# Optimization experiments

Hardware: AMD Instinct MI355X
Metric: run time of the kernel (lower is better)

Reference implementation:

```python
import jax, jax.numpy as jnp
import numpy as np

R_GAS = 8314.46261815324   # Cantera gas constant, J/(kmol K)
ONE_ATM = 101325.0
B, S, NR = 2048, 100, 800
POLY = 5


def setup_inputs() -> dict:
    key = jax.random.key(0)
    ks = jax.random.split(key, 11)
    T = jax.random.uniform(ks[0], (B, 1), minval=300.0, maxval=2500.0)
    P = ONE_ATM * jax.random.uniform(ks[1], (B, 1), minval=0.5, maxval=2.0)
    Y = jax.random.uniform(ks[2], (B, S), minval=0.01, maxval=1.0)
    TPY = jnp.concatenate([T, P, Y], axis=1)
    molecular_weights = jax.random.uniform(ks[3], (S, 1), minval=2.0, maxval=100.0)
    # NASA-7 coefficients with realistic per-column magnitudes
    scales = jnp.array([1.0, 1e-3, 1e-6, 1e-9, 1e-12, 1e3, 1.0])
    base = jnp.array([3.5, 0.0, 0.0, 0.0, 0.0, 0.0, 5.0])
    nasa_low = jax.random.normal(ks[4], (S, 7)) * scales + base
    nasa_high = jax.random.normal(ks[5], (S, 7)) * scales + base
    efficiencies_coeffs = jax.random.uniform(ks[6], (S, NR), minval=0.0, maxval=2.0)
    is_three_body = (jax.random.uniform(ks[7], (NR,)) < 0.3).astype(jnp.float32)
    # positive poly coefficients so viscosity/conductivity/diffusion stay > 0
    species_viscosities_poly = jax.random.uniform(ks[8], (POLY, S), minval=1e-6, maxval=1e-5)
    thermal_conductivity_poly = jax.random.uniform(ks[9], (POLY, S), minval=1e-4, maxval=1e-3)
    binary_diff_coeffs_poly = jax.random.uniform(ks[10], (POLY, S * S), minval=1e-7, maxval=1e-6)
    return {
        'TPY': TPY,
        'molecular_weights': molecular_weights,
        'nasa_low': nasa_low,
        'nasa_high': nasa_high,
        'efficiencies_coeffs': efficiencies_coeffs,
        'is_three_body': is_three_body,
        'species_viscosities_poly': species_viscosities_poly,
        'thermal_conductivity_poly': thermal_conductivity_poly,
        'binary_diff_coeffs_poly': binary_diff_coeffs_poly,
    }


def _forward(TPY, mw, nasa_low, nasa_high, eff, i3b, visc_poly, cond_poly, bdiff_poly):
    n_sp = mw.shape[0]
    # ---- set_states: state variables ----
    T = jnp.clip(TPY[:, 0:1], 200.0, None)            # [B,1]
    logT = jnp.log(T)
    P = TPY[:, 1:2]
    Y = jnp.clip(TPY[:, 2:], 0.0, None)
    Y = Y / Y.sum(axis=1, keepdims=True)
    mean_W = 1.0 / (Y @ (1.0 / mw))                   # [B,1]
    rho = P / R_GAS / T * mean_W                      # mass density
    X = Y * mean_W / mw.T                             # mole fractions
    C = Y * rho / mw.T                                # molar concentrations
    mask = (T <= 1000.0).astype(T.dtype)              # [B,1] NASA branch select
    # ---- cp (NASA poly) ----
    cp_T = jnp.concatenate([T**0, T, T**2, T**3, T**4], axis=1)
    cp = (cp_T @ nasa_low[:, :5].T) * mask + (cp_T @ nasa_high[:, :5].T) * (1.0 - mask)
    cp_mole = (R_GAS * cp * X).sum(axis=1)
    # ---- enthalpy ----
    H_T = jnp.concatenate([T**0, T / 2, T**2 / 3, T**3 / 4, T**4 / 5, 1.0 / T], axis=1)
    H = ((H_T @ nasa_low[:, :6].T) * mask + (H_T @ nasa_high[:, :6].T) * (1.0 - mask)) * R_GAS * T
    h = H / mw.T
    enthalpy_mass = (h * Y).sum(axis=1)
    # ---- entropy ----
    idx = jnp.array([0, 1, 2, 3, 4, 6])
    S_T = jnp.concatenate([logT, T, T**2 / 2, T**3 / 3, T**4 / 4, T**0], axis=1)
    S0 = ((S_T @ nasa_low[:, idx].T) * mask + (S_T @ nasa_high[:, idx].T) * (1.0 - mask)) * R_GAS
    S_sp = S0 - R_GAS * jnp.log(X) - R_GAS * jnp.log(P / ONE_ATM)
    s = S_sp / mw.T
    entropy_mass = (s * Y).sum(axis=1)
    # ---- third-body effective concentrations ----
    C_M = C @ eff                                     # [B,NR]
    C_M2 = C_M * i3b + (1.0 - i3b)
    # ---- update_transport: viscosity (Wilke mixing) ----
    poly_order = visc_poly.shape[0]
    trans_T = jnp.concatenate([logT**i for i in range(poly_order - 1, -1, -1)], axis=1)
    sp_visc = trans_T @ visc_poly                     # [B,S]
    Wk_over_Wj = mw @ (1.0 / mw.T)                    # [S,S]
    Wj_over_Wk = 1.0 / Wk_over_Wj
    eta_ratio = sp_visc[:, :, None] / sp_visc[:, None, :]  # [B,S,S]
    PHI = (1.0 / 2.8284271247461903) / jnp.sqrt(1.0 + Wk_over_Wj) \
          * (1.0 + jnp.sqrt(eta_ratio) * Wj_over_Wk**0.25) ** 2
    denom = jnp.einsum('bij,bj->bi', PHI, X)
    viscosities = (X * sp_visc / denom).sum(axis=1, keepdims=True)
    # ---- thermal conductivity ----
    sp_cond = trans_T @ cond_poly
    thermal_conductivity = 0.5 * ((X * sp_cond).sum(axis=1, keepdims=True)
                                  + 1.0 / (X / sp_cond).sum(axis=1, keepdims=True))
    # ---- mixture-averaged diffusion coefficients ----
    bdc = (trans_T @ bdiff_poly).reshape(-1, n_sp, n_sp)    # [B,S,S]
    X_eps = jnp.clip(X, 1e-12, None)
    XjWj = X_eps @ mw - X_eps * mw.T                        # [B,S]
    XjDjk = jnp.einsum('bj,bjk->bk', X_eps, 1.0 / bdc) \
            - X_eps / jnp.diagonal(bdc, axis1=-2, axis2=-1)
    mix_diff = XjWj / XjDjk / mean_W / P * ONE_ATM
    return jnp.concatenate([cp_mole[:, None], enthalpy_mass[:, None], entropy_mass[:, None],
                            C_M2, viscosities, thermal_conductivity, mix_diff], axis=1)


def reference(TPY, molecular_weights, nasa_low, nasa_high, efficiencies_coeffs,
              is_three_body, species_viscosities_poly, thermal_conductivity_poly,
              binary_diff_coeffs_poly):
    return _forward(TPY, molecular_weights, nasa_low, nasa_high, efficiencies_coeffs,
                    is_three_body, species_viscosities_poly, thermal_conductivity_poly,
                    binary_diff_coeffs_poly)
```

## Files before the change

### kernel.cpp

```cpp
#include <hip/hip_runtime.h>
#include <math.h>

namespace {

constexpr int S = 100;
constexpr int NR = 800;
constexpr int RPB = 8;
constexpr int NTH = 512;
constexpr int IN_COLS = 2 + S;
constexpr int OUT_COLS = 3 + NR + 2 + S;
constexpr float RGASF = 8314.46261815324f;
constexpr float ATMF = 101325.0f;

__device__ __forceinline__ float wave_sum(float v) {
#pragma unroll
  for (int off = 32; off; off >>= 1) v += __shfl_xor(v, off);
  return v;
}

__global__ __launch_bounds__(NTH)
void chem_props_kernel(const float* __restrict__ TPY,
                       const float* __restrict__ mw,
                       const float* __restrict__ nasa_low,
                       const float* __restrict__ nasa_high,
                       const float* __restrict__ eff,
                       const float* __restrict__ i3b,
                       const float* __restrict__ visc_poly,
                       const float* __restrict__ cond_poly,
                       const float* __restrict__ bdiff_poly,
                       float* __restrict__ out)
{
  __shared__ __align__(16) float Xl[S][RPB];
  __shared__ __align__(16) float u1l[S][RPB];
  __shared__ __align__(16) float u2l[S][RPB];
  __shared__ __align__(16) float viscl[S][RPB];
  __shared__ __align__(16) float svl[S][RPB];
  __shared__ __align__(16) float denoml[S][RPB];
  __shared__ __align__(16) float xjdl[S][RPB];
  __shared__ float mwl[S], imwl[S];
  __shared__ float rs_L[RPB], rs_cfac[RPB], rs_mW[RPB], rs_scale[RPB];
  __shared__ float vsum[RPB];

  const int tid = threadIdx.x;
  const int wid = tid >> 6;
  const int lane = tid & 63;
  const int row0 = blockIdx.x * RPB;
  const int rowg = row0 + wid;

  for (int idx = tid; idx < S * RPB; idx += NTH) {
    (&denoml[0][0])[idx] = 0.0f;
    (&xjdl[0][0])[idx] = 0.0f;
  }
  if (tid < RPB) vsum[tid] = 0.0f;
  if (tid < S) {
    float m = mw[tid];
    mwl[tid] = m;
    imwl[tid] = 1.0f / m;
  }
  __syncthreads();

  {
    const float* rowp = TPY + (size_t)rowg * IN_COLS;
    float T = fmaxf(rowp[0], 200.0f);
    float P = rowp[1];
    float L = logf(T);
    float T2 = T * T, T3 = T2 * T, T4 = T2 * T2;
    float invT = 1.0f / T;

    int sA = lane, sB = lane + 64;
    bool hasB = (sB < S);
    float y0 = fmaxf(rowp[2 + sA], 0.0f);
    float y1 = hasB ? fmaxf(rowp[2 + sB], 0.0f) : 0.0f;
    float im0 = imwl[sA];
    float im1 = hasB ? imwl[sB] : 0.0f;

    float ysum = wave_sum(y0 + y1);
    float invy = 1.0f / ysum;
    float sw = wave_sum(y0 * im0 + y1 * im1) * invy;
    float mW = 1.0f / sw;
    float cfac = P / (RGASF * T);
    float lnP = logf(P * (1.0f / ATMF));

    const float* nasa = (T <= 1000.0f) ? nasa_low : nasa_high;

    float cpx = 0.0f, hy = 0.0f, sy = 0.0f, condA = 0.0f, condB = 0.0f;
#pragma unroll
    for (int t = 0; t < 2; ++t) {
      int s = (t == 0) ? sA : sB;
      if (s < S) {
        float yn = ((t == 0) ? y0 : y1) * invy;
        float im = (t == 0) ? im0 : im1;
        float x = fmaxf(yn * mW * im, 1e-12f);
        const float* a = nasa + s * 7;
        float a0 = a[0], a1 = a[1], a2 = a[2], a3 = a[3],
              a4 = a[4], a5 = a[5], a6 = a[6];
        float cp = a0 + a1 * T + a2 * T2 + a3 * T3 + a4 * T4;
        float Ht = a0 + 0.5f * a1 * T + (1.0f / 3.0f) * a2 * T2
                 + 0.25f * a3 * T3 + 0.2f * a4 * T4 + a5 * invT;
        float S0r = a0 * L + a1 * T + 0.5f * a2 * T2
                  + (1.0f / 3.0f) * a3 * T3 + 0.25f * a4 * T4 + a6;
        cpx += cp * x;
        hy += Ht * im * yn;
        sy += (S0r - logf(x) - lnP) * im * yn;

        float v = visc_poly[0 * S + s];
        v = fmaf(v, L, visc_poly[1 * S + s]);
        v = fmaf(v, L, visc_poly[2 * S + s]);
        v = fmaf(v, L, visc_poly[3 * S + s]);
        v = fmaf(v, L, visc_poly[4 * S + s]);
        float c = cond_poly[0 * S + s];
        c = fmaf(c, L, cond_poly[1 * S + s]);
        c = fmaf(c, L, cond_poly[2 * S + s]);
        c = fmaf(c, L, cond_poly[3 * S + s]);
        c = fmaf(c, L, cond_poly[4 * S + s]);
        condA += x * c;
        condB += x / c;
        float sv = sqrtf(v);
        Xl[s][wid] = x;
        viscl[s][wid] = v;
        svl[s][wid] = sv;
        u1l[s][wid] = x / sv;
        u2l[s][wid] = x / v;
      }
    }
    float scp = wave_sum(cpx);
    float sh = wave_sum(hy);
    float ss = wave_sum(sy);
    float sca = wave_sum(condA);
    float scb = wave_sum(condB);
    if (lane == 0) {
      float* orow = out + (size_t)rowg * OUT_COLS;
      orow[0] = RGASF * scp;
      orow[1] = RGASF * T * sh;
      orow[2] = RGASF * ss;
      orow[3 + NR + 1] = 0.5f * (sca + 1.0f / scb);
      rs_L[wid] = L;
      rs_cfac[wid] = cfac;
      rs_mW[wid] = mW;
      rs_scale[wid] = ATMF / (mW * P);
    }
  }
  __syncthreads();

  for (int q = tid; q < NR; q += NTH) {
    float acc[RPB];
#pragma unroll
    for (int b = 0; b < RPB; ++b) acc[b] = 0.0f;
    for (int s = 0; s < S; ++s) {
      float e = eff[s * NR + q];
      float xv[RPB];
      *(float4*)&xv[0] = *(const float4*)&Xl[s][0];
      *(float4*)&xv[4] = *(const float4*)&Xl[s][4];
#pragma unroll
      for (int b = 0; b < RPB; ++b) acc[b] = fmaf(xv[b], e, acc[b]);
    }
    float t3 = i3b[q];
    float base = 1.0f - t3;
#pragma unroll
    for (int b = 0; b < RPB; ++b) {
      float cm = acc[b] * rs_cfac[b];
      out[(size_t)(row0 + b) * OUT_COLS + 3 + q] = fmaf(cm, t3, base);
    }
  }

  if (tid < 500) {
    const int i = tid % 100;
    const int kg = tid / 100;
    const float mwi = mwl[i];
    const float imwi = imwl[i];
    float d0[RPB], d1[RPB], d2[RPB];
#pragma unroll
    for (int b = 0; b < RPB; ++b) { d0[b] = 0; d1[b] = 0; d2[b] = 0; }
    const int k0 = kg * 20;
    for (int k = k0; k < k0 + 20; ++k) {
      float mwk = mwl[k];
      float A = 0.35355339059327373f *
                __builtin_amdgcn_rsqf(1.0f + mwi * imwl[k]);
      float B4 = sqrtf(sqrtf(mwk * imwi));
      float m1 = A * B4, m2 = m1 * B4;
      float xv[RPB], u1v[RPB], u2v[RPB];
      *(float4*)&xv[0] = *(const float4*)&Xl[k][0];
      *(float4*)&xv[4] = *(const float4*)&Xl[k][4];
      *(float4*)&u1v[0] = *(const float4*)&u1l[k][0];
      *(float4*)&u1v[4] = *(const float4*)&u1l[k][4];
      *(float4*)&u2v[0] = *(const float4*)&u2l[k][0];
      *(float4*)&u2v[4] = *(const float4*)&u2l[k][4];
#pragma unroll
      for (int b = 0; b < RPB; ++b) {
        d0[b] = fmaf(A, xv[b], d0[b]);
        d1[b] = fmaf(m1, u1v[b], d1[b]);
        d2[b] = fmaf(m2, u2v[b], d2[b]);
      }
    }
#pragma unroll
    for (int b = 0; b < RPB; ++b) {
      float pden = d0[b] + 2.0f * svl[i][b] * d1[b] + viscl[i][b] * d2[b];
      atomicAdd(&denoml[i][b], pden);
    }
  }
  __syncthreads();

  if (tid < 800) {
    const int i = tid % 100;
    const int b = tid / 100;
    float contrib = Xl[i][b] * viscl[i][b] / denoml[i][b];
    atomicAdd(&vsum[b], contrib);
  }
  if (tid < 500) {
    const int k = tid % 100;
    const int jg = tid / 100;
    float Lb[RPB];
#pragma unroll
    for (int b = 0; b < RPB; ++b) Lb[b] = rs_L[b];
    float acc[RPB];
#pragma unroll
    for (int b = 0; b < RPB; ++b) acc[b] = 0.0f;
    const int j0 = jg * 20;
    for (int j = j0; j < j0 + 20; ++j) {
      if (j == k) continue;
      float c0 = bdiff_poly[0 * 10000 + j * 100 + k];
      float c1 = bdiff_poly[1 * 10000 + j * 100 + k];
      float c2 = bdiff_poly[2 * 10000 + j * 100 + k];
      float c3 = bdiff_poly[3 * 10000 + j * 100 + k];
      float c4 = bdiff_poly[4 * 10000 + j * 100 + k];
      float xv[RPB];
      *(float4*)&xv[0] = *(const float4*)&Xl[j][0];
      *(float4*)&xv[4] = *(const float4*)&Xl[j][4];
#pragma unroll
      for (int b = 0; b < RPB; ++b) {
        float p = fmaf(c0, Lb[b], c1);
        p = fmaf(p, Lb[b], c2);
        p = fmaf(p, Lb[b], c3);
        p = fmaf(p, Lb[b], c4);
        acc[b] = fmaf(xv[b], __builtin_amdgcn_rcpf(p), acc[b]);
      }
    }
#pragma unroll
    for (int b = 0; b < RPB; ++b) atomicAdd(&xjdl[k][b], acc[b]);
  }
  __syncthreads();

  if (tid < RPB) {
    out[(size_t)(row0 + tid) * OUT_COLS + 3 + NR] = vsum[tid];
  }
  if (tid < 800) {
    const int k = tid % 100;
    const int b = tid / 100;
    float num = rs_mW[b] - Xl[k][b] * mwl[k];
    float md = num / xjdl[k][b] * rs_scale[b];
    out[(size_t)(row0 + b) * OUT_COLS + 3 + NR + 2 + k] = md;
  }
}

}

extern "C" void kernel_launch(void* const* d_in, const int* in_sizes, int n_in,
                              void* d_out, int out_size, void* d_ws, size_t ws_size,
                              hipStream_t stream) {
  const float* TPY        = (const float*)d_in[0];
  const float* mwp        = (const float*)d_in[1];
  const float* nasa_low   = (const float*)d_in[2];
  const float* nasa_high  = (const float*)d_in[3];
  const float* eff        = (const float*)d_in[4];
  const float* i3b        = (const float*)d_in[5];
  const float* visc_poly  = (const float*)d_in[6];
  const float* cond_poly  = (const float*)d_in[7];
  const float* bdiff_poly = (const float*)d_in[8];
  float* out = (float*)d_out;

  const int B = 2048;
  dim3 grid(B / RPB);
  chem_props_kernel<<<grid, NTH, 0, stream>>>(
      TPY, mwp, nasa_low, nasa_high, eff, i3b,
      visc_poly, cond_poly, bdiff_poly, out);
}
```

Baseline: 111.5 us.

## Halve rows per block and split species across two waves per row

Rows per block drop from 8 to 4, which doubles the grid, and each row's 100 species are split across two waves whose partial sums are combined through shared memory. The third-body loop gives each thread two adjacent reactions and reads them with float2 loads; fast __logf intrinsics and small unroll pragmas are also added. The aim is better CU occupancy and latency hiding, since the old launch had about one block per CU. The cost is that the efficiency matrix and poly tables are re-read by twice as many blocks, there are extra syncs, and __logf is slightly less accurate.

```diff
diff --git a/kernel.cpp b/kernel.cpp
--- a/kernel.cpp
+++ b/kernel.cpp
@@ -5,7 +5,7 @@
 
 constexpr int S = 100;
 constexpr int NR = 800;
-constexpr int RPB = 8;
+constexpr int RPB = 4;
 constexpr int NTH = 512;
 constexpr int IN_COLS = 2 + S;
 constexpr int OUT_COLS = 3 + NR + 2 + S;
@@ -38,14 +38,15 @@
   __shared__ __align__(16) float denoml[S][RPB];
   __shared__ __align__(16) float xjdl[S][RPB];
   __shared__ float mwl[S], imwl[S];
-  __shared__ float rs_L[RPB], rs_cfac[RPB], rs_mW[RPB], rs_scale[RPB];
+  __shared__ float pa[8][2];
+  __shared__ float pb[8][5];
+  __shared__ float rs_L[RPB], rs_cfac[RPB], rs_mW[RPB], rs_scale[RPB], rs_T[RPB];
   __shared__ float vsum[RPB];
 
   const int tid = threadIdx.x;
   const int wid = tid >> 6;
   const int lane = tid & 63;
   const int row0 = blockIdx.x * RPB;
-  const int rowg = row0 + wid;
 
   for (int idx = tid; idx < S * RPB; idx += NTH) {
     (&denoml[0][0])[idx] = 0.0f;
@@ -60,68 +61,68 @@
   __syncthreads();
 
   {
+    const int row = wid & 3;
+    const int half = wid >> 2;
+    const int rowg = row0 + row;
     const float* rowp = TPY + (size_t)rowg * IN_COLS;
     float T = fmaxf(rowp[0], 200.0f);
     float P = rowp[1];
-    float L = logf(T);
+    float L = __logf(T);
     float T2 = T * T, T3 = T2 * T, T4 = T2 * T2;
     float invT = 1.0f / T;
 
-    int sA = lane, sB = lane + 64;
-    bool hasB = (sB < S);
-    float y0 = fmaxf(rowp[2 + sA], 0.0f);
-    float y1 = hasB ? fmaxf(rowp[2 + sB], 0.0f) : 0.0f;
-    float im0 = imwl[sA];
-    float im1 = hasB ? imwl[sB] : 0.0f;
-
-    float ysum = wave_sum(y0 + y1);
+    int s = half * 64 + lane;
+    bool valid = (s < S);
+    float y = valid ? fmaxf(rowp[2 + s], 0.0f) : 0.0f;
+    float im = valid ? imwl[s] : 0.0f;
+
+    float py = wave_sum(y);
+    float pw = wave_sum(y * im);
+    if (lane == 0) { pa[wid][0] = py; pa[wid][1] = pw; }
+    __syncthreads();
+    float ysum = pa[row][0] + pa[row + 4][0];
+    float wsum = pa[row][1] + pa[row + 4][1];
     float invy = 1.0f / ysum;
-    float sw = wave_sum(y0 * im0 + y1 * im1) * invy;
-    float mW = 1.0f / sw;
+    float mW = ysum / wsum;
     float cfac = P / (RGASF * T);
-    float lnP = logf(P * (1.0f / ATMF));
+    float lnP = __logf(P * (1.0f / ATMF));
 
     const float* nasa = (T <= 1000.0f) ? nasa_low : nasa_high;
 
     float cpx = 0.0f, hy = 0.0f, sy = 0.0f, condA = 0.0f, condB = 0.0f;
-#pragma unroll
-    for (int t = 0; t < 2; ++t) {
-      int s = (t == 0) ? sA : sB;
-      if (s < S) {
-        float yn = ((t == 0) ? y0 : y1) * invy;
-        float im = (t == 0) ? im0 : im1;
-        float x = fmaxf(yn * mW * im, 1e-12f);
-        const float* a = nasa + s * 7;
-        float a0 = a[0], a1 = a[1], a2 = a[2], a3 = a[3],
-              a4 = a[4], a5 = a[5], a6 = a[6];
-        float cp = a0 + a1 * T + a2 * T2 + a3 * T3 + a4 * T4;
-        float Ht = a0 + 0.5f * a1 * T + (1.0f / 3.0f) * a2 * T2
-                 + 0.25f * a3 * T3 + 0.2f * a4 * T4 + a5 * invT;
-        float S0r = a0 * L + a1 * T + 0.5f * a2 * T2
-                  + (1.0f / 3.0f) * a3 * T3 + 0.25f * a4 * T4 + a6;
-        cpx += cp * x;
-        hy += Ht * im * yn;
-        sy += (S0r - logf(x) - lnP) * im * yn;
-
-        float v = visc_poly[0 * S + s];
-        v = fmaf(v, L, visc_poly[1 * S + s]);
-        v = fmaf(v, L, visc_poly[2 * S + s]);
-        v = fmaf(v, L, visc_poly[3 * S + s]);
-        v = fmaf(v, L, visc_poly[4 * S + s]);
-        float c = cond_poly[0 * S + s];
-        c = fmaf(c, L, cond_poly[1 * S + s]);
-        c = fmaf(c, L, cond_poly[2 * S + s]);
-        c = fmaf(c, L, cond_poly[3 * S + s]);
-        c = fmaf(c, L, cond_poly[4 * S + s]);
-        condA += x * c;
-        condB += x / c;
-        float sv = sqrtf(v);
-        Xl[s][wid] = x;
-        viscl[s][wid] = v;
-        svl[s][wid] = sv;
-        u1l[s][wid] = x / sv;
-        u2l[s][wid] = x / v;
-      }
+    if (valid) {
+      float yn = y * invy;
+      float x = fmaxf(yn * mW * im, 1e-12f);
+      const float* a = nasa + s * 7;
+      float a0 = a[0], a1 = a[1], a2 = a[2], a3 = a[3],
+            a4 = a[4], a5 = a[5], a6 = a[6];
+      float cp = a0 + a1 * T + a2 * T2 + a3 * T3 + a4 * T4;
+      float Ht = a0 + 0.5f * a1 * T + (1.0f / 3.0f) * a2 * T2
+               + 0.25f * a3 * T3 + 0.2f * a4 * T4 + a5 * invT;
+      float S0r = a0 * L + a1 * T + 0.5f * a2 * T2
+                + (1.0f / 3.0f) * a3 * T3 + 0.25f * a4 * T4 + a6;
+      cpx = cp * x;
+      hy = Ht * im * yn;
+      sy = (S0r - __logf(x) - lnP) * im * yn;
+
+      float v = visc_poly[0 * S + s];
+      v = fmaf(v, L, visc_poly[1 * S + s]);
+      v = fmaf(v, L, visc_poly[2 * S + s]);
+      v = fmaf(v, L, visc_poly[3 * S + s]);
+      v = fmaf(v, L, visc_poly[4 * S + s]);
+      float c = cond_poly[0 * S + s];
+      c = fmaf(c, L, cond_poly[1 * S + s]);
+      c = fmaf(c, L, cond_poly[2 * S + s]);
+      c = fmaf(c, L, cond_poly[3 * S + s]);
+      c = fmaf(c, L, cond_poly[4 * S + s]);
+      condA = x * c;
+      condB = x / c;
+      float sv = sqrtf(v);
+      Xl[s][row] = x;
+      viscl[s][row] = v;
+      svl[s][row] = sv;
+      u1l[s][row] = x / sv;
+      u2l[s][row] = x / v;
     }
     float scp = wave_sum(cpx);
     float sh = wave_sum(hy);
@@ -129,37 +130,57 @@
     float sca = wave_sum(condA);
     float scb = wave_sum(condB);
     if (lane == 0) {
-      float* orow = out + (size_t)rowg * OUT_COLS;
-      orow[0] = RGASF * scp;
-      orow[1] = RGASF * T * sh;
-      orow[2] = RGASF * ss;
-      orow[3 + NR + 1] = 0.5f * (sca + 1.0f / scb);
-      rs_L[wid] = L;
-      rs_cfac[wid] = cfac;
-      rs_mW[wid] = mW;
-      rs_scale[wid] = ATMF / (mW * P);
-    }
-  }
-  __syncthreads();
-
-  for (int q = tid; q < NR; q += NTH) {
-    float acc[RPB];
-#pragma unroll
-    for (int b = 0; b < RPB; ++b) acc[b] = 0.0f;
+      pb[wid][0] = scp; pb[wid][1] = sh; pb[wid][2] = ss;
+      pb[wid][3] = sca; pb[wid][4] = scb;
+      if (half == 0) {
+        rs_L[row] = L;
+        rs_T[row] = T;
+        rs_cfac[row] = cfac;
+        rs_mW[row] = mW;
+        rs_scale[row] = ATMF / (mW * P);
+      }
+    }
+  }
+  __syncthreads();
+
+  if (tid < RPB) {
+    const int row = tid;
+    float scp = pb[row][0] + pb[row + 4][0];
+    float sh  = pb[row][1] + pb[row + 4][1];
+    float ss  = pb[row][2] + pb[row + 4][2];
+    float sca = pb[row][3] + pb[row + 4][3];
+    float scb = pb[row][4] + pb[row + 4][4];
+    float* orow = out + (size_t)(row0 + row) * OUT_COLS;
+    orow[0] = RGASF * scp;
+    orow[1] = RGASF * rs_T[row] * sh;
+    orow[2] = RGASF * ss;
+    orow[3 + NR + 1] = 0.5f * (sca + 1.0f / scb);
+  }
+
+  if (tid < 400) {
+    const int q0 = 2 * tid;
+    float acc[2 * RPB];
+#pragma unroll
+    for (int b = 0; b < 2 * RPB; ++b) acc[b] = 0.0f;
+#pragma unroll 4
     for (int s = 0; s < S; ++s) {
-      float e = eff[s * NR + q];
+      float2 e = *(const float2*)&eff[s * NR + q0];
       float xv[RPB];
       *(float4*)&xv[0] = *(const float4*)&Xl[s][0];
-      *(float4*)&xv[4] = *(const float4*)&Xl[s][4];
-#pragma unroll
-      for (int b = 0; b < RPB; ++b) acc[b] = fmaf(xv[b], e, acc[b]);
-    }
-    float t3 = i3b[q];
-    float base = 1.0f - t3;
+#pragma unroll
+      for (int b = 0; b < RPB; ++b) {
+        acc[b] = fmaf(xv[b], e.x, acc[b]);
+        acc[RPB + b] = fmaf(xv[b], e.y, acc[RPB + b]);
+      }
+    }
+    float2 t3 = *(const float2*)&i3b[q0];
+    float base0 = 1.0f - t3.x, base1 = 1.0f - t3.y;
 #pragma unroll
     for (int b = 0; b < RPB; ++b) {
-      float cm = acc[b] * rs_cfac[b];
-      out[(size_t)(row0 + b) * OUT_COLS + 3 + q] = fmaf(cm, t3, base);
+      float cf = rs_cfac[b];
+      float* op = out + (size_t)(row0 + b) * OUT_COLS + 3 + q0;
+      op[0] = fmaf(acc[b] * cf, t3.x, base0);
+      op[1] = fmaf(acc[RPB + b] * cf, t3.y, base1);
     }
   }
 
@@ -172,6 +193,7 @@
 #pragma unroll
     for (int b = 0; b < RPB; ++b) { d0[b] = 0; d1[b] = 0; d2[b] = 0; }
     const int k0 = kg * 20;
+#pragma unroll 2
     for (int k = k0; k < k0 + 20; ++k) {
       float mwk = mwl[k];
       float A = 0.35355339059327373f *
@@ -180,11 +202,8 @@
       float m1 = A * B4, m2 = m1 * B4;
       float xv[RPB], u1v[RPB], u2v[RPB];
       *(float4*)&xv[0] = *(const float4*)&Xl[k][0];
-      *(float4*)&xv[4] = *(const float4*)&Xl[k][4];
       *(float4*)&u1v[0] = *(const float4*)&u1l[k][0];
-      *(float4*)&u1v[4] = *(const float4*)&u1l[k][4];
       *(float4*)&u2v[0] = *(const float4*)&u2l[k][0];
-      *(float4*)&u2v[4] = *(const float4*)&u2l[k][4];
 #pragma unroll
       for (int b = 0; b < RPB; ++b) {
         d0[b] = fmaf(A, xv[b], d0[b]);
@@ -200,7 +219,7 @@
   }
   __syncthreads();
 
-  if (tid < 800) {
+  if (tid < 100 * RPB) {
     const int i = tid % 100;
     const int b = tid / 100;
     float contrib = Xl[i][b] * viscl[i][b] / denoml[i][b];
@@ -216,6 +235,7 @@
 #pragma unroll
     for (int b = 0; b < RPB; ++b) acc[b] = 0.0f;
     const int j0 = jg * 20;
+#pragma unroll 2
     for (int j = j0; j < j0 + 20; ++j) {
       if (j == k) continue;
       float c0 = bdiff_poly[0 * 10000 + j * 100 + k];
@@ -225,7 +245,6 @@
       float c4 = bdiff_poly[4 * 10000 + j * 100 + k];
       float xv[RPB];
       *(float4*)&xv[0] = *(const float4*)&Xl[j][0];
-      *(float4*)&xv[4] = *(const float4*)&Xl[j][4];
 #pragma unroll
       for (int b = 0; b < RPB; ++b) {
         float p = fmaf(c0, Lb[b], c1);
@@ -243,7 +262,7 @@
   if (tid < RPB) {
     out[(size_t)(row0 + tid) * OUT_COLS + 3 + NR] = vsum[tid];
   }
-  if (tid < 800) {
+  if (tid < 100 * RPB) {
     const int k = tid % 100;
     const int b = tid / 100;
     float num = rs_mW[b] - Xl[k][b] * mwl[k];
```

New measurement: 105.4 us. -5.4%, faster.

## Split fused kernel into per-row stage and job-specialized worker blocks

Applied to the files above, without the earlier changes.

Replaces the single monolithic kernel with two launches. A stage kernel computes the per-row thermo state and writes X, viscosity and related terms to the workspace. A worker kernel then launches seven specialized blocks per 8-row tile: four for the three-body efficiencies matmul, one for the viscosity denominator, and two for diffusion halves. The aim is more parallelism and occupancy, since each block now does one job instead of running phases serially. The cost is a workspace round trip, an extra launch, and redundant X loads. It also uses fast intrinsics (__logf, exp2-based fourth root, rcp/rsq approximations), which may change accuracy slightly.

```diff
diff --git a/kernel.cpp b/kernel.cpp
--- a/kernel.cpp
+++ b/kernel.cpp
@@ -5,250 +5,304 @@
 
 constexpr int S = 100;
 constexpr int NR = 800;
-constexpr int RPB = 8;
-constexpr int NTH = 512;
+constexpr int RPT = 8;
 constexpr int IN_COLS = 2 + S;
 constexpr int OUT_COLS = 3 + NR + 2 + S;
 constexpr float RGASF = 8314.46261815324f;
 constexpr float ATMF = 101325.0f;
 
+constexpr size_t OFF_X  = 0;
+constexpr size_t OFF_U1 = 204800;
+constexpr size_t OFF_U2 = 409600;
+constexpr size_t OFF_V  = 614400;
+constexpr size_t OFF_RS = 819200;
+
 __device__ __forceinline__ float wave_sum(float v) {
 #pragma unroll
   for (int off = 32; off; off >>= 1) v += __shfl_xor(v, off);
   return v;
 }
 
-__global__ __launch_bounds__(NTH)
-void chem_props_kernel(const float* __restrict__ TPY,
-                       const float* __restrict__ mw,
-                       const float* __restrict__ nasa_low,
-                       const float* __restrict__ nasa_high,
-                       const float* __restrict__ eff,
-                       const float* __restrict__ i3b,
-                       const float* __restrict__ visc_poly,
-                       const float* __restrict__ cond_poly,
-                       const float* __restrict__ bdiff_poly,
-                       float* __restrict__ out)
+__device__ __forceinline__ float elem(const float4& v, int i) {
+  return ((const float*)&v)[i];
+}
+
+__global__ __launch_bounds__(512)
+void stage_a_kernel(const float* __restrict__ TPY,
+                    const float* __restrict__ mw,
+                    const float* __restrict__ nasa_low,
+                    const float* __restrict__ nasa_high,
+                    const float* __restrict__ visc_poly,
+                    const float* __restrict__ cond_poly,
+                    float* __restrict__ ws,
+                    float* __restrict__ out)
 {
-  __shared__ __align__(16) float Xl[S][RPB];
-  __shared__ __align__(16) float u1l[S][RPB];
-  __shared__ __align__(16) float u2l[S][RPB];
-  __shared__ __align__(16) float viscl[S][RPB];
-  __shared__ __align__(16) float svl[S][RPB];
-  __shared__ __align__(16) float denoml[S][RPB];
-  __shared__ __align__(16) float xjdl[S][RPB];
-  __shared__ float mwl[S], imwl[S];
-  __shared__ float rs_L[RPB], rs_cfac[RPB], rs_mW[RPB], rs_scale[RPB];
-  __shared__ float vsum[RPB];
-
+  __shared__ float imw[S];
   const int tid = threadIdx.x;
   const int wid = tid >> 6;
   const int lane = tid & 63;
-  const int row0 = blockIdx.x * RPB;
-  const int rowg = row0 + wid;
-
-  for (int idx = tid; idx < S * RPB; idx += NTH) {
-    (&denoml[0][0])[idx] = 0.0f;
-    (&xjdl[0][0])[idx] = 0.0f;
-  }
-  if (tid < RPB) vsum[tid] = 0.0f;
-  if (tid < S) {
-    float m = mw[tid];
-    mwl[tid] = m;
-    imwl[tid] = 1.0f / m;
-  }
+  if (tid < S) imw[tid] = 1.0f / mw[tid];
   __syncthreads();
 
-  {
-    const float* rowp = TPY + (size_t)rowg * IN_COLS;
-    float T = fmaxf(rowp[0], 200.0f);
-    float P = rowp[1];
-    float L = logf(T);
-    float T2 = T * T, T3 = T2 * T, T4 = T2 * T2;
-    float invT = 1.0f / T;
-
-    int sA = lane, sB = lane + 64;
-    bool hasB = (sB < S);
-    float y0 = fmaxf(rowp[2 + sA], 0.0f);
-    float y1 = hasB ? fmaxf(rowp[2 + sB], 0.0f) : 0.0f;
-    float im0 = imwl[sA];
-    float im1 = hasB ? imwl[sB] : 0.0f;
-
-    float ysum = wave_sum(y0 + y1);
-    float invy = 1.0f / ysum;
-    float sw = wave_sum(y0 * im0 + y1 * im1) * invy;
-    float mW = 1.0f / sw;
-    float cfac = P / (RGASF * T);
-    float lnP = logf(P * (1.0f / ATMF));
-
-    const float* nasa = (T <= 1000.0f) ? nasa_low : nasa_high;
-
-    float cpx = 0.0f, hy = 0.0f, sy = 0.0f, condA = 0.0f, condB = 0.0f;
-#pragma unroll
-    for (int t = 0; t < 2; ++t) {
-      int s = (t == 0) ? sA : sB;
-      if (s < S) {
-        float yn = ((t == 0) ? y0 : y1) * invy;
-        float im = (t == 0) ? im0 : im1;
-        float x = fmaxf(yn * mW * im, 1e-12f);
-        const float* a = nasa + s * 7;
-        float a0 = a[0], a1 = a[1], a2 = a[2], a3 = a[3],
-              a4 = a[4], a5 = a[5], a6 = a[6];
-        float cp = a0 + a1 * T + a2 * T2 + a3 * T3 + a4 * T4;
-        float Ht = a0 + 0.5f * a1 * T + (1.0f / 3.0f) * a2 * T2
-                 + 0.25f * a3 * T3 + 0.2f * a4 * T4 + a5 * invT;
-        float S0r = a0 * L + a1 * T + 0.5f * a2 * T2
-                  + (1.0f / 3.0f) * a3 * T3 + 0.25f * a4 * T4 + a6;
-        cpx += cp * x;
-        hy += Ht * im * yn;
-        sy += (S0r - logf(x) - lnP) * im * yn;
-
-        float v = visc_poly[0 * S + s];
-        v = fmaf(v, L, visc_poly[1 * S + s]);
-        v = fmaf(v, L, visc_poly[2 * S + s]);
-        v = fmaf(v, L, visc_poly[3 * S + s]);
-        v = fmaf(v, L, visc_poly[4 * S + s]);
-        float c = cond_poly[0 * S + s];
-        c = fmaf(c, L, cond_poly[1 * S + s]);
-        c = fmaf(c, L, cond_poly[2 * S + s]);
-        c = fmaf(c, L, cond_poly[3 * S + s]);
-        c = fmaf(c, L, cond_poly[4 * S + s]);
-        condA += x * c;
-        condB += x / c;
-        float sv = sqrtf(v);
-        Xl[s][wid] = x;
-        viscl[s][wid] = v;
-        svl[s][wid] = sv;
-        u1l[s][wid] = x / sv;
-        u2l[s][wid] = x / v;
-      }
-    }
-    float scp = wave_sum(cpx);
-    float sh = wave_sum(hy);
-    float ss = wave_sum(sy);
-    float sca = wave_sum(condA);
-    float scb = wave_sum(condB);
-    if (lane == 0) {
-      float* orow = out + (size_t)rowg * OUT_COLS;
-      orow[0] = RGASF * scp;
-      orow[1] = RGASF * T * sh;
-      orow[2] = RGASF * ss;
-      orow[3 + NR + 1] = 0.5f * (sca + 1.0f / scb);
-      rs_L[wid] = L;
-      rs_cfac[wid] = cfac;
-      rs_mW[wid] = mW;
-      rs_scale[wid] = ATMF / (mW * P);
-    }
-  }
+  const int row = blockIdx.x * 8 + wid;
+  const float* rowp = TPY + (size_t)row * IN_COLS;
+  float T = fmaxf(rowp[0], 200.0f);
+  float P = rowp[1];
+  float L = __logf(T);
+  float T2 = T * T, T3 = T2 * T, T4 = T2 * T2;
+  float invT = 1.0f / T;
+
+  int sA = lane, sB = lane + 64;
+  bool hasB = (sB < S);
+  float y0 = fmaxf(rowp[2 + sA], 0.0f);
+  float y1 = hasB ? fmaxf(rowp[2 + sB], 0.0f) : 0.0f;
+  float im0 = imw[sA];
+  float im1 = hasB ? imw[sB] : 0.0f;
+
+  float ysum = wave_sum(y0 + y1);
+  float invy = 1.0f / ysum;
+  float wsum = wave_sum(y0 * im0 + y1 * im1);
+  float mW = ysum / wsum;
+  float cfac = P / (RGASF * T);
+  float lnP = __logf(P * (1.0f / ATMF));
+  const float* nasa = (T <= 1000.0f) ? nasa_low : nasa_high;
+
+  float cpx = 0.0f, hy = 0.0f, sy = 0.0f, condA = 0.0f, condB = 0.0f;
+#pragma unroll
+  for (int t = 0; t < 2; ++t) {
+    int s = t ? sB : sA;
+    if (s < S) {
+      float y = t ? y1 : y0;
+      float im = t ? im1 : im0;
+      float yn = y * invy;
+      float x = fmaxf(yn * mW * im, 1e-12f);
+      const float* a = nasa + s * 7;
+      float a0 = a[0], a1 = a[1], a2 = a[2], a3 = a[3],
+            a4 = a[4], a5 = a[5], a6 = a[6];
+      float cp = a0 + a1 * T + a2 * T2 + a3 * T3 + a4 * T4;
+      float Ht = a0 + 0.5f * a1 * T + (1.0f / 3.0f) * a2 * T2
+               + 0.25f * a3 * T3 + 0.2f * a4 * T4 + a5 * invT;
+      float S0r = a0 * L + a1 * T + 0.5f * a2 * T2
+                + (1.0f / 3.0f) * a3 * T3 + 0.25f * a4 * T4 + a6;
+      cpx += cp * x;
+      hy += Ht * im * yn;
+      sy += (S0r - __logf(x) - lnP) * im * yn;
+
+      float v = visc_poly[0 * S + s];
+      v = fmaf(v, L, visc_poly[1 * S + s]);
+      v = fmaf(v, L, visc_poly[2 * S + s]);
+      v = fmaf(v, L, visc_poly[3 * S + s]);
+      v = fmaf(v, L, visc_poly[4 * S + s]);
+      float c = cond_poly[0 * S + s];
+      c = fmaf(c, L, cond_poly[1 * S + s]);
+      c = fmaf(c, L, cond_poly[2 * S + s]);
+      c = fmaf(c, L, cond_poly[3 * S + s]);
+      c = fmaf(c, L, cond_poly[4 * S + s]);
+      condA += x * c;
+      condB += x / c;
+
+      size_t o = (size_t)row * 100 + s;
+      ws[OFF_X + o]  = x;
+      ws[OFF_V + o]  = v;
+      ws[OFF_U1 + o] = x * __builtin_amdgcn_rsqf(v);
+      ws[OFF_U2 + o] = x * __builtin_amdgcn_rcpf(v);
+    }
+  }
+  float scp = wave_sum(cpx);
+  float sh = wave_sum(hy);
+  float ss = wave_sum(sy);
+  float sca = wave_sum(condA);
+  float scb = wave_sum(condB);
+  if (lane == 0) {
+    float* orow = out + (size_t)row * OUT_COLS;
+    orow[0] = RGASF * scp;
+    orow[1] = RGASF * T * sh;
+    orow[2] = RGASF * ss;
+    orow[3 + NR + 1] = 0.5f * (sca + 1.0f / scb);
+    float* rs = ws + OFF_RS + (size_t)row * 4;
+    rs[0] = L;
+    rs[1] = cfac;
+    rs[2] = mW;
+    rs[3] = ATMF / (mW * P);
+  }
+}
+
+__global__ __launch_bounds__(256, 6)
+void worker_kernel(const float* __restrict__ eff,
+                   const float* __restrict__ i3b,
+                   const float* __restrict__ bdiff,
+                   const float* __restrict__ mw,
+                   const float* __restrict__ ws,
+                   float* __restrict__ out)
+{
+  __shared__ __align__(16) float X8[S][RPT];
+  __shared__ __align__(16) float U18[S][RPT];
+  __shared__ __align__(16) float U28[S][RPT];
+  __shared__ __align__(16) float V8[S][RPT];
+  __shared__ float rs8[RPT][4];
+  __shared__ float mwl[S], ilmx[S], ilmy[S];
+  __shared__ __align__(16) float den[S][RPT];
+  __shared__ __align__(16) float xjd[50][RPT];
+  __shared__ float psum[2][RPT];
+
+  const int t = threadIdx.x;
+  const int bid = blockIdx.x;
+  const int rt = bid / 7;
+  const int job = bid - rt * 7;
+  const int row0 = rt * RPT;
+
+  const float* wsX = ws + OFF_X + (size_t)row0 * 100;
+  for (int idx = t; idx < 800; idx += 256)
+    X8[idx % 100][idx / 100] = wsX[idx];
+  if (job == 4) {
+    const float* w1 = ws + OFF_U1 + (size_t)row0 * 100;
+    const float* w2 = ws + OFF_U2 + (size_t)row0 * 100;
+    const float* wv = ws + OFF_V + (size_t)row0 * 100;
+    for (int idx = t; idx < 800; idx += 256) {
+      U18[idx % 100][idx / 100] = w1[idx];
+      U28[idx % 100][idx / 100] = w2[idx];
+      V8[idx % 100][idx / 100] = wv[idx];
+      (&den[0][0])[idx] = 0.0f;
+    }
+  }
+  if (job >= 5 && t < 50 * RPT) (&xjd[0][0])[t] = 0.0f;
+  if (t < S) {
+    float m = mw[t];
+    mwl[t] = m;
+    ilmx[t] = 1.0f / m;
+    ilmy[t] = __log2f(m);
+  }
+  if (t < RPT * 4) (&rs8[0][0])[t] = ws[OFF_RS + (size_t)row0 * 4 + t];
   __syncthreads();
 
-  for (int q = tid; q < NR; q += NTH) {
-    float acc[RPB];
-#pragma unroll
-    for (int b = 0; b < RPB; ++b) acc[b] = 0.0f;
-    for (int s = 0; s < S; ++s) {
-      float e = eff[s * NR + q];
-      float xv[RPB];
-      *(float4*)&xv[0] = *(const float4*)&Xl[s][0];
-      *(float4*)&xv[4] = *(const float4*)&Xl[s][4];
-#pragma unroll
-      for (int b = 0; b < RPB; ++b) acc[b] = fmaf(xv[b], e, acc[b]);
-    }
-    float t3 = i3b[q];
-    float base = 1.0f - t3;
-#pragma unroll
-    for (int b = 0; b < RPB; ++b) {
-      float cm = acc[b] * rs_cfac[b];
-      out[(size_t)(row0 + b) * OUT_COLS + 3 + q] = fmaf(cm, t3, base);
-    }
-  }
-
-  if (tid < 500) {
-    const int i = tid % 100;
-    const int kg = tid / 100;
-    const float mwi = mwl[i];
-    const float imwi = imwl[i];
-    float d0[RPB], d1[RPB], d2[RPB];
-#pragma unroll
-    for (int b = 0; b < RPB; ++b) { d0[b] = 0; d1[b] = 0; d2[b] = 0; }
-    const int k0 = kg * 20;
-    for (int k = k0; k < k0 + 20; ++k) {
-      float mwk = mwl[k];
-      float A = 0.35355339059327373f *
-                __builtin_amdgcn_rsqf(1.0f + mwi * imwl[k]);
-      float B4 = sqrtf(sqrtf(mwk * imwi));
-      float m1 = A * B4, m2 = m1 * B4;
-      float xv[RPB], u1v[RPB], u2v[RPB];
-      *(float4*)&xv[0] = *(const float4*)&Xl[k][0];
-      *(float4*)&xv[4] = *(const float4*)&Xl[k][4];
-      *(float4*)&u1v[0] = *(const float4*)&u1l[k][0];
-      *(float4*)&u1v[4] = *(const float4*)&u1l[k][4];
-      *(float4*)&u2v[0] = *(const float4*)&u2l[k][0];
-      *(float4*)&u2v[4] = *(const float4*)&u2l[k][4];
-#pragma unroll
-      for (int b = 0; b < RPB; ++b) {
-        d0[b] = fmaf(A, xv[b], d0[b]);
-        d1[b] = fmaf(m1, u1v[b], d1[b]);
-        d2[b] = fmaf(m2, u2v[b], d2[b]);
-      }
-    }
-#pragma unroll
-    for (int b = 0; b < RPB; ++b) {
-      float pden = d0[b] + 2.0f * svl[i][b] * d1[b] + viscl[i][b] * d2[b];
-      atomicAdd(&denoml[i][b], pden);
-    }
-  }
-  __syncthreads();
-
-  if (tid < 800) {
-    const int i = tid % 100;
-    const int b = tid / 100;
-    float contrib = Xl[i][b] * viscl[i][b] / denoml[i][b];
-    atomicAdd(&vsum[b], contrib);
-  }
-  if (tid < 500) {
-    const int k = tid % 100;
-    const int jg = tid / 100;
-    float Lb[RPB];
-#pragma unroll
-    for (int b = 0; b < RPB; ++b) Lb[b] = rs_L[b];
-    float acc[RPB];
-#pragma unroll
-    for (int b = 0; b < RPB; ++b) acc[b] = 0.0f;
-    const int j0 = jg * 20;
-    for (int j = j0; j < j0 + 20; ++j) {
-      if (j == k) continue;
-      float c0 = bdiff_poly[0 * 10000 + j * 100 + k];
-      float c1 = bdiff_poly[1 * 10000 + j * 100 + k];
-      float c2 = bdiff_poly[2 * 10000 + j * 100 + k];
-      float c3 = bdiff_poly[3 * 10000 + j * 100 + k];
-      float c4 = bdiff_poly[4 * 10000 + j * 100 + k];
-      float xv[RPB];
-      *(float4*)&xv[0] = *(const float4*)&Xl[j][0];
-      *(float4*)&xv[4] = *(const float4*)&Xl[j][4];
-#pragma unroll
-      for (int b = 0; b < RPB; ++b) {
-        float p = fmaf(c0, Lb[b], c1);
-        p = fmaf(p, Lb[b], c2);
-        p = fmaf(p, Lb[b], c3);
-        p = fmaf(p, Lb[b], c4);
-        acc[b] = fmaf(xv[b], __builtin_amdgcn_rcpf(p), acc[b]);
-      }
-    }
-#pragma unroll
-    for (int b = 0; b < RPB; ++b) atomicAdd(&xjdl[k][b], acc[b]);
-  }
-  __syncthreads();
-
-  if (tid < RPB) {
-    out[(size_t)(row0 + tid) * OUT_COLS + 3 + NR] = vsum[tid];
-  }
-  if (tid < 800) {
-    const int k = tid % 100;
-    const int b = tid / 100;
-    float num = rs_mW[b] - Xl[k][b] * mwl[k];
-    float md = num / xjdl[k][b] * rs_scale[b];
-    out[(size_t)(row0 + b) * OUT_COLS + 3 + NR + 2 + k] = md;
+  if (job < 4) {
+    if (t < 200) {
+      const int q = job * 200 + t;
+      float acc[RPT];
+#pragma unroll
+      for (int r = 0; r < RPT; ++r) acc[r] = 0.0f;
+#pragma unroll 4
+      for (int s = 0; s < S; ++s) {
+        float e = eff[(size_t)s * NR + q];
+        float4 xa = *(const float4*)&X8[s][0];
+        float4 xb = *(const float4*)&X8[s][4];
+#pragma unroll
+        for (int r = 0; r < 4; ++r) {
+          acc[r] = fmaf(elem(xa, r), e, acc[r]);
+          acc[4 + r] = fmaf(elem(xb, r), e, acc[4 + r]);
+        }
+      }
+      float t3 = i3b[q];
+      float base = 1.0f - t3;
+#pragma unroll
+      for (int r = 0; r < RPT; ++r)
+        out[(size_t)(row0 + r) * OUT_COLS + 3 + q] =
+            fmaf(acc[r] * rs8[r][1], t3, base);
+    }
+  } else if (job == 4) {
+    if (t < 200) {
+      const int i = t % 100;
+      const int kg = t / 100;
+      const float mwi = mwl[i];
+      const float lmi = ilmy[i];
+      float d0[RPT], d1[RPT], d2[RPT];
+#pragma unroll
+      for (int r = 0; r < RPT; ++r) { d0[r] = 0; d1[r] = 0; d2[r] = 0; }
+      const int k0 = kg * 50;
+#pragma unroll 2
+      for (int k = k0; k < k0 + 50; ++k) {
+        float A = 0.35355339059327373f *
+                  __builtin_amdgcn_rsqf(1.0f + mwi * ilmx[k]);
+        float B4 = __builtin_amdgcn_exp2f(0.25f * (ilmy[k] - lmi));
+        float m1 = A * B4, m2 = m1 * B4;
+        float4 xa = *(const float4*)&X8[k][0];
+        float4 xb = *(const float4*)&X8[k][4];
+        float4 u1a = *(const float4*)&U18[k][0];
+        float4 u1b = *(const float4*)&U18[k][4];
+        float4 u2a = *(const float4*)&U28[k][0];
+        float4 u2b = *(const float4*)&U28[k][4];
+#pragma unroll
+        for (int r = 0; r < 4; ++r) {
+          d0[r] = fmaf(A, elem(xa, r), d0[r]);
+          d0[4 + r] = fmaf(A, elem(xb, r), d0[4 + r]);
+          d1[r] = fmaf(m1, elem(u1a, r), d1[r]);
+          d1[4 + r] = fmaf(m1, elem(u1b, r), d1[4 + r]);
+          d2[r] = fmaf(m2, elem(u2a, r), d2[r]);
+          d2[4 + r] = fmaf(m2, elem(u2b, r), d2[4 + r]);
+        }
+      }
+#pragma unroll
+      for (int r = 0; r < RPT; ++r) {
+        float vi = V8[i][r];
+        float pden = d0[r] + 2.0f * sqrtf(vi) * d1[r] + vi * d2[r];
+        atomicAdd(&den[i][r], pden);
+      }
+    }
+    __syncthreads();
+    if (t < 128) {
+      float c8[RPT];
+#pragma unroll
+      for (int r = 0; r < RPT; ++r) c8[r] = 0.0f;
+      if (t < 100) {
+#pragma unroll
+        for (int r = 0; r < RPT; ++r)
+          c8[r] = X8[t][r] * V8[t][r] * __builtin_amdgcn_rcpf(den[t][r]);
+      }
+#pragma unroll
+      for (int r = 0; r < RPT; ++r) c8[r] = wave_sum(c8[r]);
+      if ((t & 63) == 0) {
+#pragma unroll
+        for (int r = 0; r < RPT; ++r) psum[t >> 6][r] = c8[r];
+      }
+    }
+    __syncthreads();
+    if (t < RPT)
+      out[(size_t)(row0 + t) * OUT_COLS + 3 + NR] = psum[0][t] + psum[1][t];
+  } else {
+    const int koff = (job - 5) * 50;
+    if (t < 250) {
+      const int kk = t % 50;
+      const int jg = t / 50;
+      const int k = koff + kk;
+      const int j0 = jg * 20;
+      float Lb[RPT], acc8[RPT];
+#pragma unroll
+      for (int r = 0; r < RPT; ++r) { Lb[r] = rs8[r][0]; acc8[r] = 0.0f; }
+      const float* bp = bdiff + k;
+#pragma unroll 2
+      for (int j = j0; j < j0 + 20; ++j) {
+        float c0 = bp[j * 100];
+        float c1 = bp[10000 + j * 100];
+        float c2 = bp[20000 + j * 100];
+        float c3 = bp[30000 + j * 100];
+        float c4 = bp[40000 + j * 100];
+        float4 xa = *(const float4*)&X8[j][0];
+        float4 xb = *(const float4*)&X8[j][4];
+        const bool diag = (j == k);
+#pragma unroll
+        for (int r = 0; r < RPT; ++r) {
+          float p = fmaf(c0, Lb[r], c1);
+          p = fmaf(p, Lb[r], c2);
+          p = fmaf(p, Lb[r], c3);
+          p = fmaf(p, Lb[r], c4);
+          float rr = diag ? 0.0f : __builtin_amdgcn_rcpf(p);
+          float xv = (r < 4) ? elem(xa, r) : elem(xb, r - 4);
+          acc8[r] = fmaf(xv, rr, acc8[r]);
+        }
+      }
+#pragma unroll
+      for (int r = 0; r < RPT; ++r) atomicAdd(&xjd[kk][r], acc8[r]);
+    }
+    __syncthreads();
+    if (t < 50 * RPT) {
+      const int kk = t % 50;
+      const int r = t / 50;
+      const int k = koff + kk;
+      float tot = xjd[kk][r];
+      float num = rs8[r][2] - X8[k][r] * mwl[k];
+      out[(size_t)(row0 + r) * OUT_COLS + 3 + NR + 2 + k] =
+          num * __builtin_amdgcn_rcpf(tot) * rs8[r][3];
+    }
   }
 }
 
@@ -267,10 +321,11 @@
   const float* cond_poly  = (const float*)d_in[7];
   const float* bdiff_poly = (const float*)d_in[8];
   float* out = (float*)d_out;
+  float* ws  = (float*)d_ws;
 
   const int B = 2048;
-  dim3 grid(B / RPB);
-  chem_props_kernel<<<grid, NTH, 0, stream>>>(
-      TPY, mwp, nasa_low, nasa_high, eff, i3b,
-      visc_poly, cond_poly, bdiff_poly, out);
-}
+  stage_a_kernel<<<B / 8, 512, 0, stream>>>(
+      TPY, mwp, nasa_low, nasa_high, visc_poly, cond_poly, ws, out);
+  worker_kernel<<<(B / RPT) * 7, 256, 0, stream>>>(
+      eff, i3b, bdiff_poly, mwp, ws, out);
+}
```

After: 100.9 us. 1.11x faster.
